# Kernel tuning notes

Hardware: AMD Instinct MI355X
Metric: run time of the kernel (lower is better)

The kernel has to match this reference:

```python
import jax, jax.numpy as jnp
import numpy as np

TEMPERATURE = 0.5


def setup_inputs() -> dict:
    key = jax.random.key(0)
    k1, k2 = jax.random.split(key)
    z_i = jax.random.normal(k1, (4096, 256), dtype=jnp.float32)
    z_j = jax.random.normal(k2, (4096, 256), dtype=jnp.float32)
    return {"z_i": z_i, "z_j": z_j}


def _l2norm(x, eps=1e-12):
    n = jnp.sqrt(jnp.sum(x * x, axis=1, keepdims=True))
    return x / jnp.maximum(n, eps)


def reference(z_i, z_j):
    n = z_i.shape[0]
    zi = _l2norm(z_i)
    zj = _l2norm(z_j)
    reps = jnp.concatenate([zi, zj], axis=0)            # [2N, D], rows unit-norm
    # cosine similarity of unit vectors == dot product -> normalized GEMM
    sim = jnp.matmul(reps, reps.T)                      # [2N, 2N]
    sim_ij = jnp.diagonal(sim, offset=n)                # [N]
    sim_ji = jnp.diagonal(sim, offset=-n)               # [N]
    positives = jnp.concatenate([sim_ij, sim_ji], axis=0)  # [2N]
    mask = 1.0 - jnp.eye(2 * n, dtype=sim.dtype)
    numerator = jnp.exp(positives / TEMPERATURE)
    denominator = jnp.sum(mask * jnp.exp(sim / TEMPERATURE), axis=1)
    loss = -jnp.log(numerator / denominator)
    return jnp.mean(loss)
```

## Files before the change

### kernel.cpp

```cpp
#include <hip/hip_runtime.h>
#include <hip/hip_bf16.h>


#define D      256
#define KC     8
#define RT     2
#define PAN    32
#define NBLK   (PAN * (PAN + 1) / 2)
#define SLOTS  32
#define CEXP   2.885390081777926f
#define E2     7.38905609893065f
#define FBLK   32

typedef __bf16 bf16x8 __attribute__((ext_vector_type(8)));
typedef float  f32x4  __attribute__((ext_vector_type(4)));
typedef __attribute__((address_space(1))) const unsigned int* gas_t;
typedef __attribute__((address_space(3))) unsigned int*       las_t;

static __device__ __forceinline__ void gload_lds16(const void* g, void* l) {
    __builtin_amdgcn_global_load_lds((gas_t)(uintptr_t)g, (las_t)(uintptr_t)l, 16, 0, 0);
}

static __device__ __forceinline__ unsigned short f2bf(float x) {
    union { float f; unsigned u; } v; v.f = x;
    unsigned r = v.u + 0x7fffu + ((v.u >> 16) & 1u);
    return (unsigned short)(r >> 16);
}

#define STAGE(bufp, srcp)                                                 \
    do {                                                                  \
        const char* s_ = (const char*)(srcp);                             \
        char* d_ = (char*)(bufp);                                         \
        _Pragma("unroll")                                                 \
        for (int i_ = 0; i_ < 4; ++i_) {                                  \
            int o_   = i_ * 8192 + threadIdx.x * 16;                      \
            int row_ = o_ >> 9;                                           \
            int cb_  = o_ & 511;                                          \
            gload_lds16(s_ + row_ * 512 + (cb_ ^ ((row_ & 7) << 4)),      \
                        d_ + o_);                                         \
        }                                                                 \
    } while (0)

__global__ __launch_bounds__(64) void knorm(const float* __restrict__ zi,
                                            const float* __restrict__ zj,
                                            unsigned short* __restrict__ reps,
                                            float* __restrict__ pos, int n) {
    const int i = blockIdx.x;
    const int lane = threadIdx.x;
    const float4 a = ((const float4*)(zi + (size_t)i * D))[lane];
    const float4 b = ((const float4*)(zj + (size_t)i * D))[lane];
    float si = a.x*a.x + a.y*a.y + a.z*a.z + a.w*a.w;
    float sj = b.x*b.x + b.y*b.y + b.z*b.z + b.w*b.w;
    float sd = a.x*b.x + a.y*b.y + a.z*b.z + a.w*b.w;
    #pragma unroll
    for (int off = 32; off; off >>= 1) {
        si += __shfl_xor(si, off);
        sj += __shfl_xor(sj, off);
        sd += __shfl_xor(sd, off);
    }
    const float inv_i = 1.0f / fmaxf(sqrtf(si), 1e-12f);
    const float inv_j = 1.0f / fmaxf(sqrtf(sj), 1e-12f);
    if (lane == 0) pos[i] = sd * inv_i * inv_j;
    ushort4 pa, pb;
    pa.x = f2bf(a.x * inv_i); pa.y = f2bf(a.y * inv_i);
    pa.z = f2bf(a.z * inv_i); pa.w = f2bf(a.w * inv_i);
    pb.x = f2bf(b.x * inv_j); pb.y = f2bf(b.y * inv_j);
    pb.z = f2bf(b.z * inv_j); pb.w = f2bf(b.w * inv_j);
    ((ushort4*)(reps + (size_t)i * D))[lane]       = pa;
    ((ushort4*)(reps + (size_t)(i + n) * D))[lane] = pb;
}

__global__ __launch_bounds__(512) void krowsum(const unsigned short* __restrict__ reps,
                                               float* __restrict__ partial) {
    __shared__ unsigned short buf[2][64 * D];
    __shared__ float cs_lds[8][16][16];
    const int lane = threadIdx.x & 63;
    const int w    = threadIdx.x >> 6;
    const int lrow = lane & 15;
    const int lkb  = (lane >> 4) * 16;
    const int swz  = (lrow & 7) << 4;

    int bid = blockIdx.x, rpan = 0, rem = PAN;
    while (bid >= rem) { bid -= rem; ++rpan; --rem; }
    const int cpan = rpan + bid;
    const bool diag = (rpan == cpan);

    const char* Bb = (const char*)reps + (size_t)cpan * 256 * 512;
    STAGE(&buf[0][0], Bb);

    bf16x8 afrag[RT][KC];
    #pragma unroll
    for (int rt = 0; rt < RT; ++rt) {
        const char* ar = (const char*)reps
                       + (size_t)(rpan * 256 + w * 32 + rt * 16 + lrow) * 512 + lkb;
        #pragma unroll
        for (int kc = 0; kc < KC; ++kc)
            afrag[rt][kc] = *(const bf16x8*)(ar + kc * 64);
    }

    float rs[RT][4];
    #pragma unroll
    for (int rt = 0; rt < RT; ++rt)
        #pragma unroll
        for (int e = 0; e < 4; ++e) rs[rt][e] = 0.f;

    __syncthreads();
    int cur = 0;
    for (int c = 0; c < 4; ++c) {
        if (c < 3) STAGE(&buf[cur ^ 1][0], Bb + (size_t)(c + 1) * 32768);
        const char* bb = (const char*)&buf[cur][0];
        float cs0 = 0.f, cs1 = 0.f, cs2 = 0.f, cs3 = 0.f;
        #pragma unroll
        for (int tp = 0; tp < 2; ++tp) {
            f32x4 acc[RT][2];
            #pragma unroll
            for (int rt = 0; rt < RT; ++rt) {
                acc[rt][0] = (f32x4){0.f, 0.f, 0.f, 0.f};
                acc[rt][1] = (f32x4){0.f, 0.f, 0.f, 0.f};
            }
            #pragma unroll
            for (int kc = 0; kc < KC; ++kc) {
                const int kb = (kc * 64 + lkb) ^ swz;
                bf16x8 bf0 = *(const bf16x8*)(bb + ((tp * 2 + 0) * 16 + lrow) * 512 + kb);
                bf16x8 bf1 = *(const bf16x8*)(bb + ((tp * 2 + 1) * 16 + lrow) * 512 + kb);
                #pragma unroll
                for (int rt = 0; rt < RT; ++rt) {
                    acc[rt][0] = __builtin_amdgcn_mfma_f32_16x16x32_bf16(
                        afrag[rt][kc], bf0, acc[rt][0], 0, 0, 0);
                    acc[rt][1] = __builtin_amdgcn_mfma_f32_16x16x32_bf16(
                        afrag[rt][kc], bf1, acc[rt][1], 0, 0, 0);
                }
            }
            #pragma unroll
            for (int rt = 0; rt < RT; ++rt)
                #pragma unroll
                for (int e = 0; e < 4; ++e) {
                    float e0 = __builtin_amdgcn_exp2f(acc[rt][0][e] * CEXP);
                    float e1 = __builtin_amdgcn_exp2f(acc[rt][1][e] * CEXP);
                    rs[rt][e] += e0 + e1;
                    if (tp == 0) { cs0 += e0; cs1 += e1; }
                    else         { cs2 += e0; cs3 += e1; }
                }
        }
        if (!diag) {
            cs0 += __shfl_xor(cs0, 16); cs0 += __shfl_xor(cs0, 32);
            cs1 += __shfl_xor(cs1, 16); cs1 += __shfl_xor(cs1, 32);
            cs2 += __shfl_xor(cs2, 16); cs2 += __shfl_xor(cs2, 32);
            cs3 += __shfl_xor(cs3, 16); cs3 += __shfl_xor(cs3, 32);
            if (lane < 16) {
                cs_lds[w][c * 4 + 0][lane] = cs0;
                cs_lds[w][c * 4 + 1][lane] = cs1;
                cs_lds[w][c * 4 + 2][lane] = cs2;
                cs_lds[w][c * 4 + 3][lane] = cs3;
            }
        }
        __syncthreads();
        cur ^= 1;
    }

    #pragma unroll
    for (int rt = 0; rt < RT; ++rt)
        #pragma unroll
        for (int e = 0; e < 4; ++e)
            #pragma unroll
            for (int off = 1; off < 16; off <<= 1)
                rs[rt][e] += __shfl_xor(rs[rt][e], off);
    if ((lane & 15) == 0) {
        #pragma unroll
        for (int rt = 0; rt < RT; ++rt) {
            const int rg = rpan * 256 + w * 32 + rt * 16 + (lane >> 4) * 4;
            #pragma unroll
            for (int e = 0; e < 4; ++e)
                partial[(size_t)(rg + e) * SLOTS + cpan] = rs[rt][e];
        }
    }

    if (!diag && threadIdx.x < 256) {
        const int ct  = threadIdx.x >> 4;
        const int col = threadIdx.x & 15;
        float v = 0.f;
        #pragma unroll
        for (int ww = 0; ww < 8; ++ww) v += cs_lds[ww][ct][col];
        const int gcol = cpan * 256 + (ct >> 2) * 64 + (ct & 3) * 16 + col;
        partial[(size_t)gcol * SLOTS + rpan] = v;
    }
}

__global__ __launch_bounds__(256) void kfinal1(const float* __restrict__ partial,
                                               const float* __restrict__ pos,
                                               float* __restrict__ bsum,
                                               int twoN, int n) {
    __shared__ float red[256];
    const int r = blockIdx.x * 256 + threadIdx.x;
    float s = 0.f;
    if (r < twoN) {
        const f32x4* pr = (const f32x4*)(partial + (size_t)r * SLOTS);
        f32x4 v = pr[0];
        #pragma unroll
        for (int q = 1; q < SLOTS / 4; ++q) {
            f32x4 u = pr[q];
            v[0] += u[0]; v[1] += u[1]; v[2] += u[2]; v[3] += u[3];
        }
        float dsum = (v[0] + v[1]) + (v[2] + v[3]) - E2;
        const float p = pos[r < n ? r : r - n];
        s = logf(dsum) - 2.0f * p;
    }
    red[threadIdx.x] = s;
    __syncthreads();
    #pragma unroll
    for (int off = 128; off; off >>= 1) {
        if (threadIdx.x < off) red[threadIdx.x] += red[threadIdx.x + off];
        __syncthreads();
    }
    if (threadIdx.x == 0) bsum[blockIdx.x] = red[0];
}

__global__ __launch_bounds__(64) void kfinal2(const float* __restrict__ bsum,
                                              float* __restrict__ out, int twoN) {
    float s = threadIdx.x < FBLK ? bsum[threadIdx.x] : 0.f;
    #pragma unroll
    for (int off = 32; off; off >>= 1) s += __shfl_xor(s, off);
    if (threadIdx.x == 0) out[0] = s / (float)twoN;
}

extern "C" void kernel_launch(void* const* d_in, const int* in_sizes, int n_in,
                              void* d_out, int out_size, void* d_ws, size_t ws_size,
                              hipStream_t stream) {
    const float* zi = (const float*)d_in[0];
    const float* zj = (const float*)d_in[1];
    const int n    = in_sizes[0] / D;
    const int twoN = 2 * n;

    unsigned short* reps = (unsigned short*)d_ws;
    float* pos     = (float*)((char*)d_ws + (size_t)twoN * D * 2);
    float* partial = pos + n;
    float* bsum    = partial + (size_t)twoN * SLOTS;
    float* out     = (float*)d_out;

    knorm<<<n, 64, 0, stream>>>(zi, zj, reps, pos, n);
    krowsum<<<NBLK, 512, 0, stream>>>(reps, partial);
    kfinal1<<<FBLK, 256, 0, stream>>>(partial, pos, bsum, twoN, n);
    kfinal2<<<1, 64, 0, stream>>>(bsum, out, twoN);
}
```

Before: 56.00 us.

## Halve B staging chunks and transpose partial sums to slot-major layout

The B panel is now staged into LDS in 32-row chunks over eight iterations instead of 64-row chunks over four. This halves the LDS footprint, which could allow more blocks per CU, at the cost of twice as many barriers. The partial row-sum buffer is transposed from row-major [2N][32] to slot-major [32][2N]. This lets krowsum write row sums as vector stores and column sums contiguously, and gives the final reduction coalesced reads across threads.

```diff
diff --git a/kernel.cpp b/kernel.cpp
--- a/kernel.cpp
+++ b/kernel.cpp
@@ -7,6 +7,7 @@
 #define RT     2
 #define PAN    32
 #define NBLK   (PAN * (PAN + 1) / 2)
+#define BN     32
 #define SLOTS  32
 #define CEXP   2.885390081777926f
 #define E2     7.38905609893065f
@@ -32,7 +33,7 @@
         const char* s_ = (const char*)(srcp);                             \
         char* d_ = (char*)(bufp);                                         \
         _Pragma("unroll")                                                 \
-        for (int i_ = 0; i_ < 4; ++i_) {                                  \
+        for (int i_ = 0; i_ < 2; ++i_) {                                  \
             int o_   = i_ * 8192 + threadIdx.x * 16;                      \
             int row_ = o_ >> 9;                                           \
             int cb_  = o_ & 511;                                          \
@@ -71,8 +72,8 @@
 }
 
 __global__ __launch_bounds__(512) void krowsum(const unsigned short* __restrict__ reps,
-                                               float* __restrict__ partial) {
-    __shared__ unsigned short buf[2][64 * D];
+                                               float* __restrict__ partial, int twoN) {
+    __shared__ unsigned short buf[2][BN * D];
     __shared__ float cs_lds[8][16][16];
     const int lane = threadIdx.x & 63;
     const int w    = threadIdx.x >> 6;
@@ -106,52 +107,44 @@
 
     __syncthreads();
     int cur = 0;
-    for (int c = 0; c < 4; ++c) {
-        if (c < 3) STAGE(&buf[cur ^ 1][0], Bb + (size_t)(c + 1) * 32768);
+    for (int c = 0; c < 8; ++c) {
+        if (c < 7) STAGE(&buf[cur ^ 1][0], Bb + (size_t)(c + 1) * (BN * 512));
         const char* bb = (const char*)&buf[cur][0];
-        float cs0 = 0.f, cs1 = 0.f, cs2 = 0.f, cs3 = 0.f;
-        #pragma unroll
-        for (int tp = 0; tp < 2; ++tp) {
-            f32x4 acc[RT][2];
+        f32x4 acc[RT][2];
+        #pragma unroll
+        for (int rt = 0; rt < RT; ++rt) {
+            acc[rt][0] = (f32x4){0.f, 0.f, 0.f, 0.f};
+            acc[rt][1] = (f32x4){0.f, 0.f, 0.f, 0.f};
+        }
+        #pragma unroll
+        for (int kc = 0; kc < KC; ++kc) {
+            const int kb = (kc * 64 + lkb) ^ swz;
+            bf16x8 bf0 = *(const bf16x8*)(bb + (lrow)        * 512 + kb);
+            bf16x8 bf1 = *(const bf16x8*)(bb + (16 + lrow)   * 512 + kb);
             #pragma unroll
             for (int rt = 0; rt < RT; ++rt) {
-                acc[rt][0] = (f32x4){0.f, 0.f, 0.f, 0.f};
-                acc[rt][1] = (f32x4){0.f, 0.f, 0.f, 0.f};
+                acc[rt][0] = __builtin_amdgcn_mfma_f32_16x16x32_bf16(
+                    afrag[rt][kc], bf0, acc[rt][0], 0, 0, 0);
+                acc[rt][1] = __builtin_amdgcn_mfma_f32_16x16x32_bf16(
+                    afrag[rt][kc], bf1, acc[rt][1], 0, 0, 0);
             }
+        }
+        float cs0 = 0.f, cs1 = 0.f;
+        #pragma unroll
+        for (int rt = 0; rt < RT; ++rt)
             #pragma unroll
-            for (int kc = 0; kc < KC; ++kc) {
-                const int kb = (kc * 64 + lkb) ^ swz;
-                bf16x8 bf0 = *(const bf16x8*)(bb + ((tp * 2 + 0) * 16 + lrow) * 512 + kb);
-                bf16x8 bf1 = *(const bf16x8*)(bb + ((tp * 2 + 1) * 16 + lrow) * 512 + kb);
-                #pragma unroll
-                for (int rt = 0; rt < RT; ++rt) {
-                    acc[rt][0] = __builtin_amdgcn_mfma_f32_16x16x32_bf16(
-                        afrag[rt][kc], bf0, acc[rt][0], 0, 0, 0);
-                    acc[rt][1] = __builtin_amdgcn_mfma_f32_16x16x32_bf16(
-                        afrag[rt][kc], bf1, acc[rt][1], 0, 0, 0);
-                }
+            for (int e = 0; e < 4; ++e) {
+                float e0 = __builtin_amdgcn_exp2f(acc[rt][0][e] * CEXP);
+                float e1 = __builtin_amdgcn_exp2f(acc[rt][1][e] * CEXP);
+                rs[rt][e] += e0 + e1;
+                cs0 += e0; cs1 += e1;
             }
-            #pragma unroll
-            for (int rt = 0; rt < RT; ++rt)
-                #pragma unroll
-                for (int e = 0; e < 4; ++e) {
-                    float e0 = __builtin_amdgcn_exp2f(acc[rt][0][e] * CEXP);
-                    float e1 = __builtin_amdgcn_exp2f(acc[rt][1][e] * CEXP);
-                    rs[rt][e] += e0 + e1;
-                    if (tp == 0) { cs0 += e0; cs1 += e1; }
-                    else         { cs2 += e0; cs3 += e1; }
-                }
-        }
         if (!diag) {
             cs0 += __shfl_xor(cs0, 16); cs0 += __shfl_xor(cs0, 32);
             cs1 += __shfl_xor(cs1, 16); cs1 += __shfl_xor(cs1, 32);
-            cs2 += __shfl_xor(cs2, 16); cs2 += __shfl_xor(cs2, 32);
-            cs3 += __shfl_xor(cs3, 16); cs3 += __shfl_xor(cs3, 32);
             if (lane < 16) {
-                cs_lds[w][c * 4 + 0][lane] = cs0;
-                cs_lds[w][c * 4 + 1][lane] = cs1;
-                cs_lds[w][c * 4 + 2][lane] = cs2;
-                cs_lds[w][c * 4 + 3][lane] = cs3;
+                cs_lds[w][c * 2 + 0][lane] = cs0;
+                cs_lds[w][c * 2 + 1][lane] = cs1;
             }
         }
         __syncthreads();
@@ -169,9 +162,8 @@
         #pragma unroll
         for (int rt = 0; rt < RT; ++rt) {
             const int rg = rpan * 256 + w * 32 + rt * 16 + (lane >> 4) * 4;
-            #pragma unroll
-            for (int e = 0; e < 4; ++e)
-                partial[(size_t)(rg + e) * SLOTS + cpan] = rs[rt][e];
+            f32x4 v = {rs[rt][0], rs[rt][1], rs[rt][2], rs[rt][3]};
+            *(f32x4*)(partial + (size_t)cpan * twoN + rg) = v;
         }
     }
 
@@ -181,8 +173,8 @@
         float v = 0.f;
         #pragma unroll
         for (int ww = 0; ww < 8; ++ww) v += cs_lds[ww][ct][col];
-        const int gcol = cpan * 256 + (ct >> 2) * 64 + (ct & 3) * 16 + col;
-        partial[(size_t)gcol * SLOTS + rpan] = v;
+        const int gcol = cpan * 256 + ct * 16 + col;
+        partial[(size_t)rpan * twoN + gcol] = v;
     }
 }
 
@@ -194,16 +186,12 @@
     const int r = blockIdx.x * 256 + threadIdx.x;
     float s = 0.f;
     if (r < twoN) {
-        const f32x4* pr = (const f32x4*)(partial + (size_t)r * SLOTS);
-        f32x4 v = pr[0];
-        #pragma unroll
-        for (int q = 1; q < SLOTS / 4; ++q) {
-            f32x4 u = pr[q];
-            v[0] += u[0]; v[1] += u[1]; v[2] += u[2]; v[3] += u[3];
-        }
-        float dsum = (v[0] + v[1]) + (v[2] + v[3]) - E2;
-        const float p = pos[r < n ? r : r - n];
-        s = logf(dsum) - 2.0f * p;
+        float dsum = 0.f;
+        #pragma unroll
+        for (int p = 0; p < SLOTS; ++p) dsum += partial[(size_t)p * twoN + r];
+        dsum -= E2;
+        const float q = pos[r < n ? r : r - n];
+        s = logf(dsum) - 2.0f * q;
     }
     red[threadIdx.x] = s;
     __syncthreads();
@@ -234,11 +222,11 @@
     unsigned short* reps = (unsigned short*)d_ws;
     float* pos     = (float*)((char*)d_ws + (size_t)twoN * D * 2);
     float* partial = pos + n;
-    float* bsum    = partial + (size_t)twoN * SLOTS;
+    float* bsum    = partial + (size_t)SLOTS * twoN;
     float* out     = (float*)d_out;
 
     knorm<<<n, 64, 0, stream>>>(zi, zj, reps, pos, n);
-    krowsum<<<NBLK, 512, 0, stream>>>(reps, partial);
+    krowsum<<<NBLK, 512, 0, stream>>>(reps, partial, twoN);
     kfinal1<<<FBLK, 256, 0, stream>>>(partial, pos, bsum, twoN, n);
     kfinal2<<<1, 64, 0, stream>>>(bsum, out, twoN);
 }
```

Result: faster. 54.37 us (-2.9%).
